# Kernel optimization log

Hardware: AMD Instinct MI355X
Metric: run time of the kernel (lower is better)

Reference implementation:

```python
import jax, jax.numpy as jnp
import numpy as np

S, D, H, HD, CQ, CKV, O = 2048, 2048, 16, 128, 96, 512, 2048


def _linear_params(k, fan_in, fan_out):
    kw, kb = jax.random.split(k)
    lim = 1.0 / np.sqrt(fan_in)
    w = jax.random.uniform(kw, (fan_out, fan_in), minval=-lim, maxval=lim, dtype=jnp.float32)
    b = jax.random.uniform(kb, (fan_out,), minval=-lim, maxval=lim, dtype=jnp.float32)
    return w, b


def setup_inputs() -> dict:
    key = jax.random.key(0)
    ks = jax.random.split(key, 8)
    x = jax.random.normal(ks[0], (S, D), dtype=jnp.float32)
    # standard RoPE tables: theta_i = 10000^(-2i/hd), rotate-half layout
    pos = jnp.arange(S, dtype=jnp.float32)[:, None]              # (S, 1)
    inv_freq = 1.0 / (10000.0 ** (jnp.arange(0, HD, 2, dtype=jnp.float32) / HD))  # (HD/2,)
    ang = pos * inv_freq[None, :]                                 # (S, HD/2)
    rope_cos = jnp.concatenate([jnp.cos(ang), jnp.cos(ang)], axis=-1)  # (S, HD)
    rope_sin = jnp.concatenate([jnp.sin(ang), jnp.sin(ang)], axis=-1)  # (S, HD)
    wq_down, bq_down = _linear_params(ks[1], D, CQ)
    wq_up, bq_up = _linear_params(ks[2], CQ, H * HD)
    wkv_down, bkv_down = _linear_params(ks[3], D, CKV)
    wk_up, bk_up = _linear_params(ks[4], CKV, H * HD)
    wv_up, bv_up = _linear_params(ks[5], CKV, H * HD)
    wo, bo = _linear_params(ks[6], H * HD, O)
    return dict(x=x, rope_cos=rope_cos, rope_sin=rope_sin,
                wq_down=wq_down, bq_down=bq_down, wq_up=wq_up, bq_up=bq_up,
                wkv_down=wkv_down, bkv_down=bkv_down, wk_up=wk_up, bk_up=bk_up,
                wv_up=wv_up, bv_up=bv_up, wo=wo, bo=bo)


def _rope(xh, cos, sin):
    # xh: (S, H, hd); cos/sin: (S, hd) broadcast over heads
    half = xh.shape[-1] // 2
    x1, x2 = xh[..., :half], xh[..., half:]
    rot = jnp.concatenate([-x2, x1], axis=-1)
    return xh * cos[:, None, :] + rot * sin[:, None, :]


def reference(x, rope_cos, rope_sin, wq_down, bq_down, wq_up, bq_up,
              wkv_down, bkv_down, wk_up, bk_up, wv_up, bv_up, wo, bo):
    s = x.shape[0]
    # low-rank Q path: down then up (compressed_q_size < head_dim branch)
    c_q = x @ wq_down.T + bq_down                                  # (S, CQ)
    q = (c_q @ wq_up.T + bq_up).reshape(s, H, HD)                  # (S, H, hd)
    q = _rope(q, rope_cos, rope_sin)
    # shared compressed KV path
    c_kv = x @ wkv_down.T + bkv_down                               # (S, CKV)
    k = _rope((c_kv @ wk_up.T + bk_up).reshape(s, H, HD), rope_cos, rope_sin)
    v = (c_kv @ wv_up.T + bv_up).reshape(s, H, HD)
    # scaled dot-product attention per head (softmax in fp32 as in source)
    q = q / jnp.sqrt(jnp.asarray(HD, q.dtype))
    logits = jnp.einsum('shd,Shd->hsS', q, k)                      # (H, S, S)
    weights = jax.nn.softmax(logits.astype(jnp.float32), axis=-1).astype(logits.dtype)
    attn = jnp.einsum('hsS,Shd->shd', weights, v).reshape(s, H * HD)
    return attn @ wo.T + bo                                        # (S, O)
```

## Files before the change

kernel.cpp:

```cpp
#include <hip/hip_runtime.h>
#include <cstdint>
#include <cstddef>

typedef unsigned short u16;
typedef float f32x4 __attribute__((ext_vector_type(4)));
typedef short s16x8 __attribute__((ext_vector_type(8)));

#define DI __device__ __forceinline__

static constexpr int S_  = 2048;
static constexpr int D_  = 2048;
static constexpr int H_  = 16;
static constexpr int HD_ = 128;
static constexpr int HHD = 2048;
static constexpr int CQP = 128;
static constexpr int NCAT = 640;
static constexpr int CKV_ = 512;

DI u16 f2bf(float f) {
  unsigned u = __float_as_uint(f);
  u += 0x7fffu + ((u >> 16) & 1u);
  return (u16)(u >> 16);
}
DI float bf2f(u16 h) { return __uint_as_float(((unsigned)h) << 16); }

DI void store_c(float* C, long long i, float v) { C[i] = v; }
DI void store_c(u16* C, long long i, float v) { C[i] = f2bf(v); }

template <int CTRL>
DI float dppf(float x) {
  return __uint_as_float((unsigned)__builtin_amdgcn_mov_dpp(
      (int)__float_as_uint(x), CTRL, 0xf, 0xf, true));
}
DI float red_max16(float x) {
  x = fmaxf(x, dppf<0xB1>(x));
  x = fmaxf(x, dppf<0x4E>(x));
  x = fmaxf(x, dppf<0x141>(x));
  x = fmaxf(x, dppf<0x140>(x));
  return x;
}
DI float red_sum16(float x) {
  x += dppf<0xB1>(x);
  x += dppf<0x4E>(x);
  x += dppf<0x141>(x);
  x += dppf<0x140>(x);
  return x;
}

#define GLD16(g, l)                                                        \
  __builtin_amdgcn_global_load_lds(                                        \
      (__attribute__((address_space(1))) void*)(void*)(const void*)(g),    \
      (__attribute__((address_space(3))) void*)(l), 16, 0, 0)

template <typename OutT, int BCOL, int BROW, int BN>
__global__ __launch_bounds__(256) void gemm_bt(
    const u16* __restrict__ A, const u16* __restrict__ B, OutT* __restrict__ C,
    const float* __restrict__ bias_col, const float* __restrict__ bias_row,
    int K, int lda, int ldb, int ldc,
    long long sA, long long sB, long long sC) {
  constexpr int MI = (BN == 128) ? 4 : 2;
  constexpr int NI = 4;
  constexpr int NCH = 8 + BN / 16;
  __shared__ __align__(16) u16 As[128 * 32];
  __shared__ __align__(16) u16 Bs[BN * 32];
  const int tid  = threadIdx.x;
  const int w    = tid >> 6;
  const int lane = tid & 63;
  const int lr   = lane & 15;
  const int lq   = lane >> 4;
  const long long m0 = (long long)blockIdx.y * 128;
  const long long n0 = (long long)blockIdx.x * BN;
  A += (long long)blockIdx.z * sA;
  B += (long long)blockIdx.z * sB;
  C += (long long)blockIdx.z * sC;
  const int wr = (BN == 128) ? (w >> 1) * 64 : w * 32;
  const int wc = (BN == 128) ? (w & 1) * 64 : 0;

  f32x4 acc[MI][NI];
#pragma unroll
  for (int i = 0; i < MI; ++i)
#pragma unroll
    for (int j = 0; j < NI; ++j)
#pragma unroll
      for (int r = 0; r < 4; ++r) acc[i][j][r] = 0.f;

  const int rch = lane >> 2, cch = (lane & 3) * 8;
  const u16* gsrc[NCH / 4];
  u16* ldst[NCH / 4];
#pragma unroll
  for (int ci = 0; ci < NCH / 4; ++ci) {
    const int c = w + ci * 4;
    if (c < 8) {
      gsrc[ci] = A + (m0 + c * 16 + rch) * lda + cch;
      ldst[ci] = &As[c * 512];
    } else {
      gsrc[ci] = B + (n0 + (c - 8) * 16 + rch) * ldb + cch;
      ldst[ci] = &Bs[(c - 8) * 512];
    }
  }

  for (int kt = 0; kt < K; kt += 32) {
    __syncthreads();
#pragma unroll
    for (int ci = 0; ci < NCH / 4; ++ci) GLD16(gsrc[ci] + kt, ldst[ci]);
    __syncthreads();

    s16x8 af[MI], bfr[NI];
#pragma unroll
    for (int tm = 0; tm < MI; ++tm)
      af[tm] = *(const s16x8*)&As[(wr + tm * 16 + lr) * 32 + lq * 8];
#pragma unroll
    for (int tn = 0; tn < NI; ++tn)
      bfr[tn] = *(const s16x8*)&Bs[(wc + tn * 16 + lr) * 32 + lq * 8];
#pragma unroll
    for (int tm = 0; tm < MI; ++tm)
#pragma unroll
      for (int tn = 0; tn < NI; ++tn)
        acc[tm][tn] = __builtin_amdgcn_mfma_f32_16x16x32_bf16(af[tm], bfr[tn],
                                                              acc[tm][tn], 0, 0, 0);
  }

#pragma unroll
  for (int tm = 0; tm < MI; ++tm)
#pragma unroll
    for (int tn = 0; tn < NI; ++tn) {
      const long long col = n0 + wc + tn * 16 + lr;
      float bc = BCOL ? bias_col[col] : 0.f;
#pragma unroll
      for (int r = 0; r < 4; ++r) {
        const long long row = m0 + wr + tm * 16 + lq * 4 + r;
        float v = acc[tm][tn][r] + bc;
        if (BROW) v += bias_row[row];
        store_c(C, row * (long long)ldc + col, v);
      }
    }
}

DI void store4(float* d, long long e, float4 s) { *(float4*)(d + e) = s; }
DI void store4(u16* d, long long e, float4 s) {
  unsigned lo = (unsigned)f2bf(s.x) | ((unsigned)f2bf(s.y) << 16);
  unsigned hi = (unsigned)f2bf(s.z) | ((unsigned)f2bf(s.w) << 16);
  *(uint2*)(d + e) = make_uint2(lo, hi);
}
template <typename OutT>
__global__ __launch_bounds__(256) void combine_z(
    const float* __restrict__ p, long long zs, int nz,
    const float* __restrict__ bias, OutT* __restrict__ dst, int ldc, int n4) {
  int i = blockIdx.x * 256 + threadIdx.x;
  if (i >= n4) return;
  long long e = (long long)i * 4;
  float4 s = *(const float4*)(p + e);
  for (int z = 1; z < nz; ++z) {
    float4 t = *(const float4*)(p + (long long)z * zs + e);
    s.x += t.x; s.y += t.y; s.z += t.z; s.w += t.w;
  }
  int c = (int)(e % ldc);
  s.x += bias[c]; s.y += bias[c + 1]; s.z += bias[c + 2]; s.w += bias[c + 3];
  store4(dst, e, s);
}

__global__ __launch_bounds__(256, 1) void flash_attn(
    const u16* __restrict__ Q, const u16* __restrict__ Kg,
    const u16* __restrict__ Vt, u16* __restrict__ Og) {
  __shared__ __align__(16) u16 Ks[128 * 128];
  __shared__ __align__(16) u16 Vs[128 * 128];
  __shared__ __align__(16) u16 Ps[128 * 136];
  const int h = blockIdx.x;
  const int t = blockIdx.y;
  const int tid = threadIdx.x;
  const int w = tid >> 6, lane = tid & 63, lr = lane & 15, lq = lane >> 4;
  const int qg = t * 128 + w * 32;
  const int tr = tid >> 4;
  const int cs = (tid & 15) ^ (tr & 7);

  s16x8 qf[2][4];
#pragma unroll
  for (int mi = 0; mi < 2; ++mi)
#pragma unroll
    for (int kst = 0; kst < 4; ++kst)
      qf[mi][kst] = *(const s16x8*)&Q[(size_t)(qg + mi * 16 + lr) * HHD +
                                      h * HD_ + kst * 32 + lq * 8];

  f32x4 oacc[2][8];
  float m[2][4], l[2][4];
#pragma unroll
  for (int mi = 0; mi < 2; ++mi) {
#pragma unroll
    for (int r = 0; r < 4; ++r) { m[mi][r] = -3.0e38f; l[mi][r] = 0.f; }
#pragma unroll
    for (int f = 0; f < 8; ++f)
#pragma unroll
      for (int r = 0; r < 4; ++r) oacc[mi][f][r] = 0.f;
  }

  auto stage_k = [&](int j) {
    const u16* s0 = Kg + (size_t)(j * 128 + tr) * HHD + h * HD_ + cs * 8;
#pragma unroll
    for (int i = 0; i < 8; ++i)
      GLD16(s0 + (size_t)i * 16 * HHD, &Ks[i * 2048 + w * 512]);
  };
  auto stage_v = [&](int j) {
    const u16* s0 = Vt + (size_t)(h * 128 + tr) * S_ + j * 128 + cs * 8;
#pragma unroll
    for (int i = 0; i < 8; ++i)
      GLD16(s0 + (size_t)i * 16 * S_, &Vs[i * 2048 + w * 512]);
  };

  stage_k(0);
  stage_v(0);
  __syncthreads();

  for (int j = 0; j < 16; ++j) {
    f32x4 sacc[2][8];
#pragma unroll
    for (int mi = 0; mi < 2; ++mi)
#pragma unroll
      for (int f = 0; f < 8; ++f)
#pragma unroll
        for (int r = 0; r < 4; ++r) sacc[mi][f][r] = 0.f;
#pragma unroll
    for (int kst = 0; kst < 4; ++kst)
#pragma unroll
      for (int f = 0; f < 8; ++f) {
        s16x8 kf = *(const s16x8*)
            &Ks[(f * 16 + lr) * 128 + (((kst * 4 + lq) ^ (lr & 7)) << 3)];
        sacc[0][f] = __builtin_amdgcn_mfma_f32_16x16x32_bf16(qf[0][kst], kf,
                                                             sacc[0][f], 0, 0, 0);
        sacc[1][f] = __builtin_amdgcn_mfma_f32_16x16x32_bf16(qf[1][kst], kf,
                                                             sacc[1][f], 0, 0, 0);
      }

#pragma unroll
    for (int mi = 0; mi < 2; ++mi)
#pragma unroll
      for (int r = 0; r < 4; ++r) {
        float mx = sacc[mi][0][r];
#pragma unroll
        for (int f = 1; f < 8; ++f) mx = fmaxf(mx, sacc[mi][f][r]);
        mx = red_max16(mx);
        float mn = fmaxf(m[mi][r], mx);
        float al = __expf(m[mi][r] - mn);
        m[mi][r] = mn;
        float sum = 0.f;
#pragma unroll
        for (int f = 0; f < 8; ++f) {
          float p = __expf(sacc[mi][f][r] - mn);
          sacc[mi][f][r] = p;
          sum += p;
        }
        sum = red_sum16(sum);
        l[mi][r] = l[mi][r] * al + sum;
#pragma unroll
        for (int f = 0; f < 8; ++f) oacc[mi][f][r] *= al;
      }

#pragma unroll
    for (int mi = 0; mi < 2; ++mi)
#pragma unroll
      for (int f = 0; f < 8; ++f)
#pragma unroll
        for (int r = 0; r < 4; ++r)
          Ps[(w * 32 + mi * 16 + lq * 4 + r) * 136 + f * 16 + lr] =
              f2bf(sacc[mi][f][r]);

    __syncthreads();
    if (j < 15) stage_k(j + 1);

#pragma unroll
    for (int kst = 0; kst < 4; ++kst) {
      s16x8 pa0 = *(const s16x8*)&Ps[(w * 32 + lr) * 136 + kst * 32 + lq * 8];
      s16x8 pa1 = *(const s16x8*)&Ps[(w * 32 + 16 + lr) * 136 + kst * 32 + lq * 8];
#pragma unroll
      for (int f = 0; f < 8; ++f) {
        s16x8 vf = *(const s16x8*)
            &Vs[(f * 16 + lr) * 128 + (((kst * 4 + lq) ^ (lr & 7)) << 3)];
        oacc[0][f] = __builtin_amdgcn_mfma_f32_16x16x32_bf16(pa0, vf,
                                                             oacc[0][f], 0, 0, 0);
        oacc[1][f] = __builtin_amdgcn_mfma_f32_16x16x32_bf16(pa1, vf,
                                                             oacc[1][f], 0, 0, 0);
      }
    }
    __syncthreads();
    if (j < 15) stage_v(j + 1);
  }

#pragma unroll
  for (int mi = 0; mi < 2; ++mi) {
    float inv[4];
#pragma unroll
    for (int r = 0; r < 4; ++r) inv[r] = 1.f / l[mi][r];
#pragma unroll
    for (int f = 0; f < 8; ++f)
#pragma unroll
      for (int r = 0; r < 4; ++r)
        Og[(size_t)(qg + mi * 16 + lq * 4 + r) * HHD + h * HD_ + f * 16 + lr] =
            f2bf(oacc[mi][f][r] * inv[r]);
  }
}

__global__ __launch_bounds__(256) void cast_f32_bf16(const float* __restrict__ s,
                                                     u16* __restrict__ d, int n4) {
  int i = blockIdx.x * 256 + threadIdx.x;
  if (i >= n4) return;
  float4 f = ((const float4*)s)[i];
  unsigned lo = (unsigned)f2bf(f.x) | ((unsigned)f2bf(f.y) << 16);
  unsigned hi = (unsigned)f2bf(f.z) | ((unsigned)f2bf(f.w) << 16);
  ((uint2*)d)[i] = make_uint2(lo, hi);
}

__global__ __launch_bounds__(256) void pad_cast2d(const float* __restrict__ s,
                                                  u16* __restrict__ d, int rs, int cs,
                                                  int cd, int nd) {
  int i = blockIdx.x * 256 + threadIdx.x;
  if (i >= nd) return;
  int r = i / cd, c = i % cd;
  float v = (r < rs && c < cs) ? s[r * cs + c] : 0.f;
  d[i] = f2bf(v);
}

__global__ __launch_bounds__(256) void build_wcat(const float* __restrict__ wqd,
                                                  const float* __restrict__ wkvd,
                                                  u16* __restrict__ d) {
  int i = blockIdx.x * 256 + threadIdx.x;
  int n = i >> 11, k = i & 2047;
  float v = (n < 96) ? wqd[n * D_ + k] : (n < 128 ? 0.f : wkvd[(n - 128) * D_ + k]);
  d[i] = f2bf(v);
}
__global__ void build_bcat(const float* __restrict__ bqd,
                           const float* __restrict__ bkvd, float* __restrict__ d) {
  int i = threadIdx.x;
  d[i] = (i < 96) ? bqd[i] : (i < 128 ? 0.f : bkvd[i - 128]);
}

__global__ __launch_bounds__(256) void rope_inplace(u16* __restrict__ X,
                                                    const float* __restrict__ cs,
                                                    const float* __restrict__ sn,
                                                    float scale) {
  int id = blockIdx.x * 256 + threadIdx.x;
  int d = id & 63;
  int h = (id >> 6) & 15;
  int s = id >> 10;
  long long b = (long long)s * HHD + h * HD_ + d;
  float x1 = bf2f(X[b]), x2 = bf2f(X[b + 64]);
  int cb = s * HD_ + d;
  float o1 = (x1 * cs[cb] - x2 * sn[cb]) * scale;
  float o2 = (x2 * cs[cb + 64] + x1 * sn[cb + 64]) * scale;
  X[b] = f2bf(o1);
  X[b + 64] = f2bf(o2);
}

extern "C" void kernel_launch(void* const* d_in, const int* in_sizes, int n_in,
                              void* d_out, int out_size, void* d_ws, size_t ws_size,
                              hipStream_t stream) {
  (void)in_sizes; (void)n_in; (void)out_size; (void)ws_size;
  const float* x        = (const float*)d_in[0];
  const float* rc       = (const float*)d_in[1];
  const float* rs       = (const float*)d_in[2];
  const float* wq_down  = (const float*)d_in[3];
  const float* bq_down  = (const float*)d_in[4];
  const float* wq_up    = (const float*)d_in[5];
  const float* bq_up    = (const float*)d_in[6];
  const float* wkv_down = (const float*)d_in[7];
  const float* bkv_down = (const float*)d_in[8];
  const float* wk_up    = (const float*)d_in[9];
  const float* bk_up    = (const float*)d_in[10];
  const float* wv_up    = (const float*)d_in[11];
  const float* bv_up    = (const float*)d_in[12];
  const float* wo       = (const float*)d_in[13];
  const float* bo       = (const float*)d_in[14];
  float* out = (float*)d_out;

  char* ws = (char*)d_ws;
  size_t off = 0;
  auto alloc = [&](size_t bytes) -> void* {
    off = (off + 255) & ~(size_t)255;
    void* p = ws + off;
    off += bytes;
    return p;
  };

  u16* xb      = (u16*)alloc((size_t)S_ * D_ * 2);
  u16* wcat    = (u16*)alloc((size_t)NCAT * D_ * 2);
  float* bcat  = (float*)alloc(NCAT * 4);
  u16* wqu     = (u16*)alloc((size_t)HHD * CQP * 2);
  u16* wku     = (u16*)alloc((size_t)HHD * CKV_ * 2);
  u16* wvu     = (u16*)alloc((size_t)HHD * CKV_ * 2);
  u16* wob     = (u16*)alloc((size_t)D_ * HHD * 2);
  u16* ccat    = (u16*)alloc((size_t)S_ * NCAT * 2);
  float* pcat  = (float*)alloc((size_t)4 * S_ * NCAT * 4);
  u16* qb      = (u16*)alloc((size_t)S_ * HHD * 2);
  u16* kb      = (u16*)alloc((size_t)S_ * HHD * 2);
  u16* vT      = (u16*)alloc((size_t)HHD * S_ * 2);
  u16* attnb   = (u16*)alloc((size_t)S_ * HHD * 2);
  float* pout  = (float*)alloc((size_t)2 * S_ * D_ * 4);

  cast_f32_bf16<<<(S_ * D_ / 4 + 255) / 256, 256, 0, stream>>>(x, xb, S_ * D_ / 4);
  build_wcat<<<(NCAT * D_) / 256, 256, 0, stream>>>(wq_down, wkv_down, wcat);
  build_bcat<<<1, NCAT, 0, stream>>>(bq_down, bkv_down, bcat);
  pad_cast2d<<<(HHD * CQP + 255) / 256, 256, 0, stream>>>(wq_up, wqu, HHD, 96, CQP, HHD * CQP);
  cast_f32_bf16<<<(HHD * CKV_ / 4 + 255) / 256, 256, 0, stream>>>(wk_up, wku, HHD * CKV_ / 4);
  cast_f32_bf16<<<(HHD * CKV_ / 4 + 255) / 256, 256, 0, stream>>>(wv_up, wvu, HHD * CKV_ / 4);
  cast_f32_bf16<<<(D_ * HHD / 4 + 255) / 256, 256, 0, stream>>>(wo, wob, D_ * HHD / 4);

  gemm_bt<float, 0, 0, 64><<<dim3(NCAT / 64, 16, 4), 256, 0, stream>>>(
      xb, wcat, pcat, nullptr, nullptr, 512, D_, D_, NCAT,
      512, 512, (long long)S_ * NCAT);
  combine_z<u16><<<(S_ * NCAT / 4 + 255) / 256, 256, 0, stream>>>(
      pcat, (long long)S_ * NCAT, 4, bcat, ccat, NCAT, S_ * NCAT / 4);

  gemm_bt<u16, 1, 0, 128><<<dim3(16, 16, 1), 256, 0, stream>>>(
      ccat, wqu, qb, bq_up, nullptr, CQP, NCAT, CQP, HHD, 0, 0, 0);
  gemm_bt<u16, 1, 0, 128><<<dim3(16, 16, 1), 256, 0, stream>>>(
      ccat + CQP, wku, kb, bk_up, nullptr, CKV_, NCAT, CKV_, HHD, 0, 0, 0);
  gemm_bt<u16, 0, 1, 128><<<dim3(16, 16, 1), 256, 0, stream>>>(
      wvu, ccat + CQP, vT, nullptr, bv_up, CKV_, CKV_, NCAT, S_, 0, 0, 0);

  rope_inplace<<<(S_ * H_ * 64) / 256, 256, 0, stream>>>(qb, rc, rs, 0.08838834764831845f);
  rope_inplace<<<(S_ * H_ * 64) / 256, 256, 0, stream>>>(kb, rc, rs, 1.0f);

  flash_attn<<<dim3(H_, S_ / 128, 1), 256, 0, stream>>>(qb, kb, vT, attnb);

  gemm_bt<float, 0, 0, 128><<<dim3(16, 16, 2), 256, 0, stream>>>(
      attnb, wob, pout, nullptr, nullptr, 1024, HHD, HHD, D_,
      1024, 1024, (long long)S_ * D_);
  combine_z<float><<<(S_ * D_ / 4 + 255) / 256, 256, 0, stream>>>(
      pout, (long long)S_ * D_, 2, bo, out, D_, S_ * D_ / 4);
}
```

Measured before the change: 316.1 us.

## Double-buffer GEMM tiles, widen attention blocks, fuse prep and rope kernels

The GEMM kernel gains double-buffered shared tiles, so the next K-slice loads while MFMAs run on the current one, with one barrier per iteration instead of two. Flash attention moves to 512 threads per block, with each wave owning 16 query rows instead of 32, aiming at more waves per CU and lower register pressure. The weight and input casts are merged into a single prep kernel, the two RoPE launches into one, and the output projection drops split-K in favour of a single GEMM with fused bias. Together these cut launch count and extra memory passes, at the cost of doubled GEMM shared memory and less parallelism in the output GEMM.

```diff
diff --git a/kernel.cpp b/kernel.cpp
--- a/kernel.cpp
+++ b/kernel.cpp
@@ -61,8 +61,9 @@
   constexpr int MI = (BN == 128) ? 4 : 2;
   constexpr int NI = 4;
   constexpr int NCH = 8 + BN / 16;
-  __shared__ __align__(16) u16 As[128 * 32];
-  __shared__ __align__(16) u16 Bs[BN * 32];
+  constexpr int NC4 = NCH / 4;
+  __shared__ __align__(16) u16 As[2 * 128 * 32];
+  __shared__ __align__(16) u16 Bs[2 * BN * 32];
   const int tid  = threadIdx.x;
   const int w    = tid >> 6;
   const int lane = tid & 63;
@@ -85,39 +86,49 @@
       for (int r = 0; r < 4; ++r) acc[i][j][r] = 0.f;
 
   const int rch = lane >> 2, cch = (lane & 3) * 8;
-  const u16* gsrc[NCH / 4];
-  u16* ldst[NCH / 4];
-#pragma unroll
-  for (int ci = 0; ci < NCH / 4; ++ci) {
+  const u16* gsrc[NC4];
+  u16* ldst[NC4];
+  int bstep[NC4];
+#pragma unroll
+  for (int ci = 0; ci < NC4; ++ci) {
     const int c = w + ci * 4;
     if (c < 8) {
       gsrc[ci] = A + (m0 + c * 16 + rch) * lda + cch;
       ldst[ci] = &As[c * 512];
+      bstep[ci] = 128 * 32;
     } else {
       gsrc[ci] = B + (n0 + (c - 8) * 16 + rch) * ldb + cch;
       ldst[ci] = &Bs[(c - 8) * 512];
-    }
-  }
-
+      bstep[ci] = BN * 32;
+    }
+  }
+  auto stage = [&](int kt, int b) {
+#pragma unroll
+    for (int ci = 0; ci < NC4; ++ci) GLD16(gsrc[ci] + kt, ldst[ci] + b * bstep[ci]);
+  };
+
+  stage(0, 0);
+  int cur = 0;
   for (int kt = 0; kt < K; kt += 32) {
     __syncthreads();
-#pragma unroll
-    for (int ci = 0; ci < NCH / 4; ++ci) GLD16(gsrc[ci] + kt, ldst[ci]);
-    __syncthreads();
+    if (kt + 32 < K) stage(kt + 32, cur ^ 1);
+    const u16* Ab = &As[cur * 128 * 32];
+    const u16* Bb = &Bs[cur * BN * 32];
 
     s16x8 af[MI], bfr[NI];
 #pragma unroll
     for (int tm = 0; tm < MI; ++tm)
-      af[tm] = *(const s16x8*)&As[(wr + tm * 16 + lr) * 32 + lq * 8];
+      af[tm] = *(const s16x8*)&Ab[(wr + tm * 16 + lr) * 32 + lq * 8];
 #pragma unroll
     for (int tn = 0; tn < NI; ++tn)
-      bfr[tn] = *(const s16x8*)&Bs[(wc + tn * 16 + lr) * 32 + lq * 8];
+      bfr[tn] = *(const s16x8*)&Bb[(wc + tn * 16 + lr) * 32 + lq * 8];
 #pragma unroll
     for (int tm = 0; tm < MI; ++tm)
 #pragma unroll
       for (int tn = 0; tn < NI; ++tn)
         acc[tm][tn] = __builtin_amdgcn_mfma_f32_16x16x32_bf16(af[tm], bfr[tn],
                                                               acc[tm][tn], 0, 0, 0);
+    cur ^= 1;
   }
 
 #pragma unroll
@@ -159,51 +170,47 @@
   store4(dst, e, s);
 }
 
-__global__ __launch_bounds__(256, 1) void flash_attn(
+__global__ __launch_bounds__(512, 2) void flash_attn(
     const u16* __restrict__ Q, const u16* __restrict__ Kg,
     const u16* __restrict__ Vt, u16* __restrict__ Og) {
   __shared__ __align__(16) u16 Ks[128 * 128];
   __shared__ __align__(16) u16 Vs[128 * 128];
-  __shared__ __align__(16) u16 Ps[128 * 136];
+  __shared__ __align__(16) u16 Ps[128 * 132];
   const int h = blockIdx.x;
   const int t = blockIdx.y;
   const int tid = threadIdx.x;
   const int w = tid >> 6, lane = tid & 63, lr = lane & 15, lq = lane >> 4;
-  const int qg = t * 128 + w * 32;
-  const int tr = tid >> 4;
-  const int cs = (tid & 15) ^ (tr & 7);
-
-  s16x8 qf[2][4];
-#pragma unroll
-  for (int mi = 0; mi < 2; ++mi)
-#pragma unroll
-    for (int kst = 0; kst < 4; ++kst)
-      qf[mi][kst] = *(const s16x8*)&Q[(size_t)(qg + mi * 16 + lr) * HHD +
-                                      h * HD_ + kst * 32 + lq * 8];
-
-  f32x4 oacc[2][8];
-  float m[2][4], l[2][4];
-#pragma unroll
-  for (int mi = 0; mi < 2; ++mi) {
-#pragma unroll
-    for (int r = 0; r < 4; ++r) { m[mi][r] = -3.0e38f; l[mi][r] = 0.f; }
-#pragma unroll
-    for (int f = 0; f < 8; ++f)
-#pragma unroll
-      for (int r = 0; r < 4; ++r) oacc[mi][f][r] = 0.f;
-  }
+  const int qg = t * 128 + w * 16;
+  const int rsub = w * 4 + (lane >> 4);
+  const int csw  = (lane & 15) ^ (rsub & 7);
+
+  s16x8 qf[4];
+#pragma unroll
+  for (int kst = 0; kst < 4; ++kst)
+    qf[kst] = *(const s16x8*)&Q[(size_t)(qg + lr) * HHD + h * HD_ + kst * 32 + lq * 8];
+
+  f32x4 oacc[8];
+  float m[4], l[4];
+#pragma unroll
+  for (int r = 0; r < 4; ++r) { m[r] = -3.0e38f; l[r] = 0.f; }
+#pragma unroll
+  for (int f = 0; f < 8; ++f)
+#pragma unroll
+    for (int r = 0; r < 4; ++r) oacc[f][r] = 0.f;
 
   auto stage_k = [&](int j) {
-    const u16* s0 = Kg + (size_t)(j * 128 + tr) * HHD + h * HD_ + cs * 8;
-#pragma unroll
-    for (int i = 0; i < 8; ++i)
-      GLD16(s0 + (size_t)i * 16 * HHD, &Ks[i * 2048 + w * 512]);
+#pragma unroll
+    for (int i = 0; i < 4; ++i) {
+      const u16* s0 = Kg + (size_t)(j * 128 + i * 32 + rsub) * HHD + h * HD_ + csw * 8;
+      GLD16(s0, &Ks[(i * 32 + w * 4) * 128]);
+    }
   };
   auto stage_v = [&](int j) {
-    const u16* s0 = Vt + (size_t)(h * 128 + tr) * S_ + j * 128 + cs * 8;
-#pragma unroll
-    for (int i = 0; i < 8; ++i)
-      GLD16(s0 + (size_t)i * 16 * S_, &Vs[i * 2048 + w * 512]);
+#pragma unroll
+    for (int i = 0; i < 4; ++i) {
+      const u16* s0 = Vt + (size_t)(h * HD_ + i * 32 + rsub) * S_ + j * 128 + csw * 8;
+      GLD16(s0, &Vs[(i * 32 + w * 4) * 128]);
+    }
   };
 
   stage_k(0);
@@ -211,132 +218,154 @@
   __syncthreads();
 
   for (int j = 0; j < 16; ++j) {
-    f32x4 sacc[2][8];
-#pragma unroll
-    for (int mi = 0; mi < 2; ++mi)
-#pragma unroll
-      for (int f = 0; f < 8; ++f)
-#pragma unroll
-        for (int r = 0; r < 4; ++r) sacc[mi][f][r] = 0.f;
+    f32x4 sacc[8];
+#pragma unroll
+    for (int f = 0; f < 8; ++f)
+#pragma unroll
+      for (int r = 0; r < 4; ++r) sacc[f][r] = 0.f;
 #pragma unroll
     for (int kst = 0; kst < 4; ++kst)
 #pragma unroll
       for (int f = 0; f < 8; ++f) {
         s16x8 kf = *(const s16x8*)
             &Ks[(f * 16 + lr) * 128 + (((kst * 4 + lq) ^ (lr & 7)) << 3)];
-        sacc[0][f] = __builtin_amdgcn_mfma_f32_16x16x32_bf16(qf[0][kst], kf,
-                                                             sacc[0][f], 0, 0, 0);
-        sacc[1][f] = __builtin_amdgcn_mfma_f32_16x16x32_bf16(qf[1][kst], kf,
-                                                             sacc[1][f], 0, 0, 0);
+        sacc[f] = __builtin_amdgcn_mfma_f32_16x16x32_bf16(qf[kst], kf, sacc[f], 0, 0, 0);
       }
 
 #pragma unroll
-    for (int mi = 0; mi < 2; ++mi)
-#pragma unroll
-      for (int r = 0; r < 4; ++r) {
-        float mx = sacc[mi][0][r];
-#pragma unroll
-        for (int f = 1; f < 8; ++f) mx = fmaxf(mx, sacc[mi][f][r]);
-        mx = red_max16(mx);
-        float mn = fmaxf(m[mi][r], mx);
-        float al = __expf(m[mi][r] - mn);
-        m[mi][r] = mn;
-        float sum = 0.f;
-#pragma unroll
-        for (int f = 0; f < 8; ++f) {
-          float p = __expf(sacc[mi][f][r] - mn);
-          sacc[mi][f][r] = p;
-          sum += p;
-        }
-        sum = red_sum16(sum);
-        l[mi][r] = l[mi][r] * al + sum;
-#pragma unroll
-        for (int f = 0; f < 8; ++f) oacc[mi][f][r] *= al;
+    for (int r = 0; r < 4; ++r) {
+      float mx = sacc[0][r];
+#pragma unroll
+      for (int f = 1; f < 8; ++f) mx = fmaxf(mx, sacc[f][r]);
+      mx = red_max16(mx);
+      float mn = fmaxf(m[r], mx);
+      float al = __expf(m[r] - mn);
+      m[r] = mn;
+      float sum = 0.f;
+#pragma unroll
+      for (int f = 0; f < 8; ++f) {
+        float p = __expf(sacc[f][r] - mn);
+        sacc[f][r] = p;
+        sum += p;
       }
-
-#pragma unroll
-    for (int mi = 0; mi < 2; ++mi)
-#pragma unroll
-      for (int f = 0; f < 8; ++f)
-#pragma unroll
-        for (int r = 0; r < 4; ++r)
-          Ps[(w * 32 + mi * 16 + lq * 4 + r) * 136 + f * 16 + lr] =
-              f2bf(sacc[mi][f][r]);
+      sum = red_sum16(sum);
+      l[r] = l[r] * al + sum;
+#pragma unroll
+      for (int f = 0; f < 8; ++f) oacc[f][r] *= al;
+    }
+
+#pragma unroll
+    for (int f = 0; f < 8; ++f)
+#pragma unroll
+      for (int r = 0; r < 4; ++r)
+        Ps[(w * 16 + lq * 4 + r) * 132 + f * 16 + lr] = f2bf(sacc[f][r]);
 
     __syncthreads();
     if (j < 15) stage_k(j + 1);
 
 #pragma unroll
     for (int kst = 0; kst < 4; ++kst) {
-      s16x8 pa0 = *(const s16x8*)&Ps[(w * 32 + lr) * 136 + kst * 32 + lq * 8];
-      s16x8 pa1 = *(const s16x8*)&Ps[(w * 32 + 16 + lr) * 136 + kst * 32 + lq * 8];
+      s16x8 pa = *(const s16x8*)&Ps[(w * 16 + lr) * 132 + kst * 32 + lq * 8];
 #pragma unroll
       for (int f = 0; f < 8; ++f) {
         s16x8 vf = *(const s16x8*)
             &Vs[(f * 16 + lr) * 128 + (((kst * 4 + lq) ^ (lr & 7)) << 3)];
-        oacc[0][f] = __builtin_amdgcn_mfma_f32_16x16x32_bf16(pa0, vf,
-                                                             oacc[0][f], 0, 0, 0);
-        oacc[1][f] = __builtin_amdgcn_mfma_f32_16x16x32_bf16(pa1, vf,
-                                                             oacc[1][f], 0, 0, 0);
+        oacc[f] = __builtin_amdgcn_mfma_f32_16x16x32_bf16(pa, vf, oacc[f], 0, 0, 0);
       }
     }
     __syncthreads();
     if (j < 15) stage_v(j + 1);
   }
 
-#pragma unroll
-  for (int mi = 0; mi < 2; ++mi) {
-    float inv[4];
-#pragma unroll
-    for (int r = 0; r < 4; ++r) inv[r] = 1.f / l[mi][r];
-#pragma unroll
-    for (int f = 0; f < 8; ++f)
-#pragma unroll
-      for (int r = 0; r < 4; ++r)
-        Og[(size_t)(qg + mi * 16 + lq * 4 + r) * HHD + h * HD_ + f * 16 + lr] =
-            f2bf(oacc[mi][f][r] * inv[r]);
-  }
-}
-
-__global__ __launch_bounds__(256) void cast_f32_bf16(const float* __restrict__ s,
-                                                     u16* __restrict__ d, int n4) {
-  int i = blockIdx.x * 256 + threadIdx.x;
-  if (i >= n4) return;
-  float4 f = ((const float4*)s)[i];
+  float inv[4];
+#pragma unroll
+  for (int r = 0; r < 4; ++r) inv[r] = 1.f / l[r];
+#pragma unroll
+  for (int f = 0; f < 8; ++f)
+#pragma unroll
+    for (int r = 0; r < 4; ++r)
+      Og[(size_t)(qg + lq * 4 + r) * HHD + h * HD_ + f * 16 + lr] =
+          f2bf(oacc[f][r] * inv[r]);
+}
+
+DI void cast4(const float* __restrict__ s, u16* __restrict__ d, int v) {
+  float4 f = ((const float4*)s)[v];
   unsigned lo = (unsigned)f2bf(f.x) | ((unsigned)f2bf(f.y) << 16);
   unsigned hi = (unsigned)f2bf(f.z) | ((unsigned)f2bf(f.w) << 16);
-  ((uint2*)d)[i] = make_uint2(lo, hi);
-}
-
-__global__ __launch_bounds__(256) void pad_cast2d(const float* __restrict__ s,
-                                                  u16* __restrict__ d, int rs, int cs,
-                                                  int cd, int nd) {
-  int i = blockIdx.x * 256 + threadIdx.x;
-  if (i >= nd) return;
-  int r = i / cd, c = i % cd;
-  float v = (r < rs && c < cs) ? s[r * cs + c] : 0.f;
-  d[i] = f2bf(v);
-}
-
-__global__ __launch_bounds__(256) void build_wcat(const float* __restrict__ wqd,
-                                                  const float* __restrict__ wkvd,
-                                                  u16* __restrict__ d) {
-  int i = blockIdx.x * 256 + threadIdx.x;
-  int n = i >> 11, k = i & 2047;
-  float v = (n < 96) ? wqd[n * D_ + k] : (n < 128 ? 0.f : wkvd[(n - 128) * D_ + k]);
-  d[i] = f2bf(v);
-}
-__global__ void build_bcat(const float* __restrict__ bqd,
-                           const float* __restrict__ bkvd, float* __restrict__ d) {
-  int i = threadIdx.x;
-  d[i] = (i < 96) ? bqd[i] : (i < 128 ? 0.f : bkvd[i - 128]);
-}
-
-__global__ __launch_bounds__(256) void rope_inplace(u16* __restrict__ X,
-                                                    const float* __restrict__ cs,
-                                                    const float* __restrict__ sn,
-                                                    float scale) {
+  ((uint2*)d)[v] = make_uint2(lo, hi);
+}
+DI void store_bf4(u16* __restrict__ d, int i, float4 f) {
+  unsigned lo = (unsigned)f2bf(f.x) | ((unsigned)f2bf(f.y) << 16);
+  unsigned hi = (unsigned)f2bf(f.z) | ((unsigned)f2bf(f.w) << 16);
+  *(uint2*)(d + i) = make_uint2(lo, hi);
+}
+static constexpr int PV_XB   = 1048576;
+static constexpr int PV_WCAT = 327680;
+static constexpr int PV_WQU  = 65536;
+static constexpr int PV_WKU  = 262144;
+static constexpr int PV_WVU  = 262144;
+static constexpr int PV_WOB  = 1048576;
+static constexpr int PV_BCAT = 160;
+static constexpr int PV_TOT  = PV_XB + PV_WCAT + PV_WQU + PV_WKU + PV_WVU + PV_WOB + PV_BCAT;
+
+__global__ __launch_bounds__(256) void prep(
+    const float* __restrict__ x, const float* __restrict__ wqd_s,
+    const float* __restrict__ wkvd_s, const float* __restrict__ wqu_s,
+    const float* __restrict__ wku_s, const float* __restrict__ wvu_s,
+    const float* __restrict__ wo_s, const float* __restrict__ bqd_s,
+    const float* __restrict__ bkvd_s,
+    u16* __restrict__ xb, u16* __restrict__ wcat, u16* __restrict__ wqu,
+    u16* __restrict__ wku, u16* __restrict__ wvu, u16* __restrict__ wob,
+    float* __restrict__ bcat) {
+  int v = blockIdx.x * 256 + threadIdx.x;
+  if (v >= PV_TOT) return;
+  if (v < PV_XB) { cast4(x, xb, v); return; }
+  v -= PV_XB;
+  if (v < PV_WCAT) {
+    int i = v * 4, n = i >> 11, k = i & 2047;
+    float4 o = make_float4(0.f, 0.f, 0.f, 0.f);
+    if (n < 96)       o = *(const float4*)&wqd_s[n * D_ + k];
+    else if (n >= 128) o = *(const float4*)&wkvd_s[(n - 128) * D_ + k];
+    store_bf4(wcat, i, o);
+    return;
+  }
+  v -= PV_WCAT;
+  if (v < PV_WQU) {
+    int i = v * 4, r = i >> 7, c = i & 127;
+    float4 o = (c < 96) ? *(const float4*)&wqu_s[r * 96 + c]
+                        : make_float4(0.f, 0.f, 0.f, 0.f);
+    store_bf4(wqu, i, o);
+    return;
+  }
+  v -= PV_WQU;
+  if (v < PV_WKU) { cast4(wku_s, wku, v); return; }
+  v -= PV_WKU;
+  if (v < PV_WVU) { cast4(wvu_s, wvu, v); return; }
+  v -= PV_WVU;
+  if (v < PV_WOB) { cast4(wo_s, wob, v); return; }
+  v -= PV_WOB;
+  {
+    int i = v * 4;
+    float4 o;
+    float* po = &o.x;
+#pragma unroll
+    for (int jj = 0; jj < 4; ++jj) {
+      int e = i + jj;
+      po[jj] = (e < 96) ? bqd_s[e] : (e < 128 ? 0.f : bkvd_s[e - 128]);
+    }
+    *(float4*)&bcat[i] = o;
+  }
+}
+
+__global__ __launch_bounds__(256) void rope2(u16* __restrict__ qb,
+                                             u16* __restrict__ kb,
+                                             const float* __restrict__ cs,
+                                             const float* __restrict__ sn) {
   int id = blockIdx.x * 256 + threadIdx.x;
+  const bool isq = id < S_ * H_ * 64;
+  if (!isq) id -= S_ * H_ * 64;
+  u16* X = isq ? qb : kb;
+  const float scale = isq ? 0.08838834764831845f : 1.0f;
   int d = id & 63;
   int h = (id >> 6) & 15;
   int s = id >> 10;
@@ -392,15 +421,10 @@
   u16* kb      = (u16*)alloc((size_t)S_ * HHD * 2);
   u16* vT      = (u16*)alloc((size_t)HHD * S_ * 2);
   u16* attnb   = (u16*)alloc((size_t)S_ * HHD * 2);
-  float* pout  = (float*)alloc((size_t)2 * S_ * D_ * 4);
-
-  cast_f32_bf16<<<(S_ * D_ / 4 + 255) / 256, 256, 0, stream>>>(x, xb, S_ * D_ / 4);
-  build_wcat<<<(NCAT * D_) / 256, 256, 0, stream>>>(wq_down, wkv_down, wcat);
-  build_bcat<<<1, NCAT, 0, stream>>>(bq_down, bkv_down, bcat);
-  pad_cast2d<<<(HHD * CQP + 255) / 256, 256, 0, stream>>>(wq_up, wqu, HHD, 96, CQP, HHD * CQP);
-  cast_f32_bf16<<<(HHD * CKV_ / 4 + 255) / 256, 256, 0, stream>>>(wk_up, wku, HHD * CKV_ / 4);
-  cast_f32_bf16<<<(HHD * CKV_ / 4 + 255) / 256, 256, 0, stream>>>(wv_up, wvu, HHD * CKV_ / 4);
-  cast_f32_bf16<<<(D_ * HHD / 4 + 255) / 256, 256, 0, stream>>>(wo, wob, D_ * HHD / 4);
+
+  prep<<<(PV_TOT + 255) / 256, 256, 0, stream>>>(
+      x, wq_down, wkv_down, wq_up, wk_up, wv_up, wo, bq_down, bkv_down,
+      xb, wcat, wqu, wku, wvu, wob, bcat);
 
   gemm_bt<float, 0, 0, 64><<<dim3(NCAT / 64, 16, 4), 256, 0, stream>>>(
       xb, wcat, pcat, nullptr, nullptr, 512, D_, D_, NCAT,
@@ -415,14 +439,10 @@
   gemm_bt<u16, 0, 1, 128><<<dim3(16, 16, 1), 256, 0, stream>>>(
       wvu, ccat + CQP, vT, nullptr, bv_up, CKV_, CKV_, NCAT, S_, 0, 0, 0);
 
-  rope_inplace<<<(S_ * H_ * 64) / 256, 256, 0, stream>>>(qb, rc, rs, 0.08838834764831845f);
-  rope_inplace<<<(S_ * H_ * 64) / 256, 256, 0, stream>>>(kb, rc, rs, 1.0f);
-
-  flash_attn<<<dim3(H_, S_ / 128, 1), 256, 0, stream>>>(qb, kb, vT, attnb);
-
-  gemm_bt<float, 0, 0, 128><<<dim3(16, 16, 2), 256, 0, stream>>>(
-      attnb, wob, pout, nullptr, nullptr, 1024, HHD, HHD, D_,
-      1024, 1024, (long long)S_ * D_);
-  combine_z<float><<<(S_ * D_ / 4 + 255) / 256, 256, 0, stream>>>(
-      pout, (long long)S_ * D_, 2, bo, out, D_, S_ * D_ / 4);
-}
+  rope2<<<(2 * S_ * H_ * 64) / 256, 256, 0, stream>>>(qb, kb, rc, rs);
+
+  flash_attn<<<dim3(H_, S_ / 128, 1), 512, 0, stream>>>(qb, kb, vT, attnb);
+
+  gemm_bt<float, 1, 0, 128><<<dim3(16, 16, 1), 256, 0, stream>>>(
+      attnb, wob, out, bo, nullptr, HHD, HHD, HHD, D_, 0, 0, 0);
+}
```

Result: faster. 286.7 us (-9.3%).
